# Optimization experiments

Hardware: AMD Instinct MI355X
Metric: run time of the kernel (lower is better)

Reference implementation:

```python
import jax, jax.numpy as jnp
import numpy as np

N = 100000
E = 1600000
F_IN = 128
HID = 128
C = 10
NEG_SLOPE = 0.2


def setup_inputs() -> dict:
    key = jax.random.key(0)
    ks = jax.random.split(key, 12)
    x = jax.random.normal(ks[0], (N, F_IN), dtype=jnp.float32)
    edge_index = jax.random.randint(ks[1], (2, E), 0, N, dtype=jnp.int64)
    batch = jnp.zeros((N,), dtype=jnp.int64)
    s1 = 1.0 / np.sqrt(F_IN)
    s2 = 1.0 / np.sqrt(HID)
    return {
        "x": x,
        "edge_index": edge_index,
        "batch": batch,
        "W1": jax.random.normal(ks[2], (F_IN, HID), dtype=jnp.float32) * s1,
        "a_src1": jax.random.normal(ks[3], (HID,), dtype=jnp.float32) * s2,
        "a_dst1": jax.random.normal(ks[4], (HID,), dtype=jnp.float32) * s2,
        "b1": jnp.zeros((HID,), dtype=jnp.float32),
        "W2": jax.random.normal(ks[5], (HID, HID), dtype=jnp.float32) * s2,
        "a_src2": jax.random.normal(ks[6], (HID,), dtype=jnp.float32) * s2,
        "a_dst2": jax.random.normal(ks[7], (HID,), dtype=jnp.float32) * s2,
        "b2": jnp.zeros((HID,), dtype=jnp.float32),
        "Wlin": jax.random.normal(ks[8], (HID, C), dtype=jnp.float32) * s2,
        "blin": jnp.zeros((C,), dtype=jnp.float32),
    }


def gat_conv(x, src, dst, W, a_src, a_dst, b):
    # PyG GATConv, heads=1: h = xW; alpha_e = softmax_dst(leaky_relu(a_src.h[src] + a_dst.h[dst]))
    h = x @ W                                  # [N, H]
    alpha_s = h @ a_src                        # [N]
    alpha_d = h @ a_dst                        # [N]
    e = jax.nn.leaky_relu(alpha_s[src] + alpha_d[dst], NEG_SLOPE)  # [E]
    m = jax.ops.segment_max(e, dst, num_segments=N)                # per-dst max (stable softmax)
    ex = jnp.exp(e - m[dst])
    denom = jax.ops.segment_sum(ex, dst, num_segments=N)
    alpha = ex / (denom[dst] + 1e-16)          # [E]
    out = jax.ops.segment_sum(h[src] * alpha[:, None], dst, num_segments=N)
    return out + b


def reference(x, edge_index, batch, W1, a_src1, a_dst1, b1, W2, a_src2, a_dst2, b2, Wlin, blin):
    x = x.astype(jnp.float32)
    loops = jnp.arange(N, dtype=edge_index.dtype)
    src = jnp.concatenate([edge_index[0], loops])  # add_self_loops=True
    dst = jnp.concatenate([edge_index[1], loops])
    h = jax.nn.relu(gat_conv(x, src, dst, W1, a_src1, a_dst1, b1))
    h = jax.nn.relu(gat_conv(h, src, dst, W2, a_src2, a_dst2, b2))
    # dropout(p=0.5) is identity in eval mode
    return h @ Wlin + blin
```

## Files before the change

kernel.cpp:

```cpp
#include <hip/hip_runtime.h>

#define N_NODES 100000
#define N_EDGES 1600000
#define TOTE    (N_EDGES + N_NODES)
#define NEG     0.2f
#define NB      ((N_NODES + 255) >> 8)
#define BCAP    5120

typedef __attribute__((ext_vector_type(8))) short bf16x8;
typedef __attribute__((ext_vector_type(4))) float floatx4;

__device__ __forceinline__ unsigned short f2bf(float f) {
  unsigned int u = __float_as_uint(f);
  u += 0x7fffu + ((u >> 16) & 1u);
  return (unsigned short)(u >> 16);
}
__device__ __forceinline__ float bf_lo(unsigned int r) { return __uint_as_float(r << 16); }
__device__ __forceinline__ float bf_hi(unsigned int r) { return __uint_as_float(r & 0xffff0000u); }

__global__ __launch_bounds__(256) void k_wprep(const float* __restrict__ W1, const float* __restrict__ W2,
                                               unsigned short* __restrict__ B1hi, unsigned short* __restrict__ B1lo,
                                               unsigned short* __restrict__ B2hi, unsigned short* __restrict__ B2lo,
                                               int* __restrict__ bucketCnt) {
  int b = blockIdx.x;
  int t = threadIdx.x;
  if (b == 16) {
    for (int i = t; i < NB * 16; i += 256) bucketCnt[i] = 0;
    return;
  }
  const float* W = (b < 8) ? W1 : W2;
  unsigned short* Bh = (b < 8) ? B1hi : B2hi;
  unsigned short* Bl = (b < 8) ? B1lo : B2lo;
  int ntile = b & 7;
  int kq = t >> 6, lane = t & 63;
  int q = lane >> 4, m = lane & 15;
  int n = ntile * 16 + m;
  union { unsigned short us[8]; uint4 u4; } hi, lo;
#pragma unroll
  for (int j = 0; j < 8; ++j) {
    int k = kq * 32 + q * 8 + j;
    float w = W[(size_t)k * 128 + n];
    unsigned int u = __float_as_uint(w);
    hi.us[j] = (unsigned short)(u >> 16);
    float res = w - __uint_as_float(u & 0xffff0000u);
    lo.us[j] = f2bf(res);
  }
  size_t fo = ((size_t)(ntile * 4 + kq) * 64 + lane) * 8;
  *reinterpret_cast<uint4*>(Bh + fo) = hi.u4;
  *reinterpret_cast<uint4*>(Bl + fo) = lo.u4;
}

__global__ __launch_bounds__(256) void k_binA(const int* __restrict__ ei, int* __restrict__ bucketCnt,
                                              unsigned int* __restrict__ binned) {
  __shared__ int hist[NB];
  __shared__ int cur[NB];
  int t = threadIdx.x;
  for (int b = t; b < NB; b += 256) hist[b] = 0;
  __syncthreads();
  unsigned int pk[16]; int bk[16];
#pragma unroll
  for (int j = 0; j < 16; ++j) {
    int idx = blockIdx.x * 4096 + j * 256 + t;
    if (idx < N_EDGES) {
      int s = ei[idx], d = ei[N_EDGES + idx];
      bk[j] = d >> 8;
      pk[j] = ((unsigned int)s << 8) | (unsigned int)(d & 255);
      atomicAdd(&hist[bk[j]], 1);
    } else bk[j] = -1;
  }
  __syncthreads();
  for (int b = t; b < NB; b += 256) {
    int h = hist[b];
    if (h) cur[b] = b * BCAP + atomicAdd(&bucketCnt[b * 16], h);
  }
  __syncthreads();
#pragma unroll
  for (int j = 0; j < 16; ++j) {
    if (bk[j] >= 0) {
      int pos = atomicAdd(&cur[bk[j]], 1);
      binned[pos] = pk[j];
    }
  }
}

__global__ __launch_bounds__(512) void k_bin_scan(const int* __restrict__ bucketCnt,
                                                  int* __restrict__ binOffs) {
  __shared__ int sc[512];
  int t = threadIdx.x;
  int v = (t < NB) ? bucketCnt[t * 16] : 0;
  sc[t] = v; __syncthreads();
  for (int off = 1; off < 512; off <<= 1) {
    int x = (t >= off) ? sc[t - off] : 0;
    __syncthreads();
    sc[t] += x;
    __syncthreads();
  }
  int excl = sc[t] - v;
  if (t <= NB) binOffs[t] = excl;
}

__global__ __launch_bounds__(256) void k_binB(const unsigned int* __restrict__ binned,
                                              const int* __restrict__ binOffs,
                                              int* __restrict__ offs, int* __restrict__ srcs) {
  __shared__ int cnt[256];
  __shared__ int sc[256];
  __shared__ int cur[256];
  int b = blockIdx.x;
  int t = threadIdx.x;
  int node0 = b << 8;
  int nNodes = min(256, N_NODES - node0);
  int cntE = binOffs[b + 1] - binOffs[b];
  int e0 = b * BCAP, e1 = e0 + cntE;
  int base = binOffs[b] + node0;

  cnt[t] = 0; __syncthreads();
  for (int i = e0 + t; i < e1; i += 256) atomicAdd(&cnt[binned[i] & 255u], 1);
  __syncthreads();

  int v = (t < nNodes) ? cnt[t] + 1 : 0;
  sc[t] = v; __syncthreads();
  for (int off = 1; off < 256; off <<= 1) {
    int x = (t >= off) ? sc[t - off] : 0;
    __syncthreads();
    sc[t] += x;
    __syncthreads();
  }
  int excl = sc[t] - v;
  if (t < nNodes) {
    offs[node0 + t] = base + excl;
    srcs[base + excl] = node0 + t;
  }
  cur[t] = excl + 1;
  __syncthreads();

  for (int i = e0 + t; i < e1; i += 256) {
    unsigned int e = binned[i];
    int j = (int)(e & 255u);
    int s = (int)(e >> 8);
    int p = atomicAdd(&cur[j], 1);
    srcs[base + p] = s;
  }
  if (b == 0 && t == 0) offs[N_NODES] = TOTE;
}

template <bool SPLIT>
__global__ __launch_bounds__(256) void k_gemm_mfma(const void* __restrict__ Aptr,
                                                   const unsigned short* __restrict__ Bhi,
                                                   const unsigned short* __restrict__ Blo,
                                                   unsigned short* __restrict__ Cb,
                                                   const float* __restrict__ avS, const float* __restrict__ avD,
                                                   float* __restrict__ aS, float* __restrict__ aD,
                                                   float* __restrict__ slotS, float* __restrict__ slotD) {
  __shared__ unsigned short sC[64 * 136];
  __shared__ float redS[64 * 4], redD[64 * 4];
  __shared__ float mS[64], mD[64];
  int t = threadIdx.x;
  int w = t >> 6, lane = t & 63;
  int q = lane >> 4, m = lane & 15;
  int rbase = blockIdx.x * 64;

  floatx4 acc[4][2];
#pragma unroll
  for (int mt = 0; mt < 4; ++mt)
#pragma unroll
    for (int nt = 0; nt < 2; ++nt) acc[mt][nt] = (floatx4){0.f, 0.f, 0.f, 0.f};

#pragma unroll
  for (int k0 = 0; k0 < 4; ++k0) {
    bf16x8 Bh[2], Bl[2], Ah[4], Al[4];
#pragma unroll
    for (int nt = 0; nt < 2; ++nt) {
      int ntg = w * 2 + nt;
      size_t fo = ((size_t)(ntg * 4 + k0) * 64 + lane) * 8;
      Bh[nt] = *reinterpret_cast<const bf16x8*>(Bhi + fo);
      Bl[nt] = *reinterpret_cast<const bf16x8*>(Blo + fo);
    }
#pragma unroll
    for (int mt = 0; mt < 4; ++mt) {
      int row = rbase + mt * 16 + m;
      row = min(row, N_NODES - 1);
      if constexpr (SPLIT) {
        const float* ap = (const float*)Aptr + (size_t)row * 128 + k0 * 32 + q * 8;
        float4 v0 = *reinterpret_cast<const float4*>(ap);
        float4 v1 = *reinterpret_cast<const float4*>(ap + 4);
        float av[8] = {v0.x, v0.y, v0.z, v0.w, v1.x, v1.y, v1.z, v1.w};
        union { unsigned short us[8]; bf16x8 v; } uh, ul;
#pragma unroll
        for (int j = 0; j < 8; ++j) {
          unsigned int u = __float_as_uint(av[j]);
          uh.us[j] = (unsigned short)(u >> 16);
          float res = av[j] - __uint_as_float(u & 0xffff0000u);
          ul.us[j] = f2bf(res);
        }
        Ah[mt] = uh.v; Al[mt] = ul.v;
      } else {
        const unsigned short* ap = (const unsigned short*)Aptr + (size_t)row * 128 + k0 * 32 + q * 8;
        Ah[mt] = *reinterpret_cast<const bf16x8*>(ap);
      }
    }
#pragma unroll
    for (int mt = 0; mt < 4; ++mt)
#pragma unroll
      for (int nt = 0; nt < 2; ++nt) {
        acc[mt][nt] = __builtin_amdgcn_mfma_f32_16x16x32_bf16(Ah[mt], Bh[nt], acc[mt][nt], 0, 0, 0);
        acc[mt][nt] = __builtin_amdgcn_mfma_f32_16x16x32_bf16(Ah[mt], Bl[nt], acc[mt][nt], 0, 0, 0);
        if constexpr (SPLIT)
          acc[mt][nt] = __builtin_amdgcn_mfma_f32_16x16x32_bf16(Al[mt], Bh[nt], acc[mt][nt], 0, 0, 0);
      }
  }

  float avs[2], avd[2];
#pragma unroll
  for (int nt = 0; nt < 2; ++nt) {
    int c = w * 32 + nt * 16 + m;
    avs[nt] = avS[c];
    avd[nt] = avD[c];
  }
#pragma unroll
  for (int mt = 0; mt < 4; ++mt)
#pragma unroll
    for (int r = 0; r < 4; ++r) {
      float ps = acc[mt][0][r] * avs[0] + acc[mt][1][r] * avs[1];
      float pd = acc[mt][0][r] * avd[0] + acc[mt][1][r] * avd[1];
      ps += __shfl_xor(ps, 1); pd += __shfl_xor(pd, 1);
      ps += __shfl_xor(ps, 2); pd += __shfl_xor(pd, 2);
      ps += __shfl_xor(ps, 4); pd += __shfl_xor(pd, 4);
      ps += __shfl_xor(ps, 8); pd += __shfl_xor(pd, 8);
      if (m == 0) {
        int rl = mt * 16 + q * 4 + r;
        redS[rl * 4 + w] = ps;
        redD[rl * 4 + w] = pd;
      }
    }

#pragma unroll
  for (int mt = 0; mt < 4; ++mt)
#pragma unroll
    for (int nt = 0; nt < 2; ++nt)
#pragma unroll
      for (int r = 0; r < 4; ++r) {
        int rl = mt * 16 + q * 4 + r;
        int cl = w * 32 + nt * 16 + m;
        sC[rl * 136 + cl] = f2bf(acc[mt][nt][r]);
      }
  __syncthreads();

#pragma unroll
  for (int i = 0; i < 4; ++i) {
    int idx = i * 256 + t;
    int rl = idx >> 4, kk = idx & 15;
    int gr = rbase + rl;
    if (gr < N_NODES)
      *reinterpret_cast<uint4*>(Cb + (size_t)gr * 128 + kk * 8) =
          *reinterpret_cast<const uint4*>(sC + rl * 136 + kk * 8);
  }

  if (t < 64) {
    int gr = rbase + t;
    bool ok = gr < N_NODES;
    float ps = redS[t * 4] + redS[t * 4 + 1] + redS[t * 4 + 2] + redS[t * 4 + 3];
    float pd = redD[t * 4] + redD[t * 4 + 1] + redD[t * 4 + 2] + redD[t * 4 + 3];
    if (ok) { aS[gr] = ps; aD[gr] = pd; }
    mS[t] = ok ? ps : -1e30f;
    mD[t] = ok ? pd : -1e30f;
  }
  __syncthreads();
#pragma unroll
  for (int off = 32; off > 0; off >>= 1) {
    if (t < off) { mS[t] = fmaxf(mS[t], mS[t + off]); mD[t] = fmaxf(mD[t], mD[t + off]); }
    __syncthreads();
  }
  if (t == 0) { slotS[blockIdx.x] = mS[0]; slotD[blockIdx.x] = mD[0]; }
}

__global__ __launch_bounds__(256) void k_gmax(const float* __restrict__ slotS,
                                              const float* __restrict__ slotD,
                                              int n, float* __restrict__ gMh) {
  __shared__ float sS[256], sD[256];
  int t = threadIdx.x;
  float ms = -1e30f, md = -1e30f;
  for (int i = t; i < n; i += 256) { ms = fmaxf(ms, slotS[i]); md = fmaxf(md, slotD[i]); }
  sS[t] = ms; sD[t] = md;
  __syncthreads();
#pragma unroll
  for (int off = 128; off > 0; off >>= 1) {
    if (t < off) { sS[t] = fmaxf(sS[t], sS[t + off]); sD[t] = fmaxf(sD[t], sD[t + off]); }
    __syncthreads();
  }
  if (t == 0) {
    float M = sS[0] + sD[0];
    gMh[0] = (M > 0.f) ? M : NEG * M;
  }
}

#define FMA8(E, R)                                     \
  do {                                                 \
    acc[0] += (E) * bf_lo((R).x); acc[1] += (E) * bf_hi((R).x); \
    acc[2] += (E) * bf_lo((R).y); acc[3] += (E) * bf_hi((R).y); \
    acc[4] += (E) * bf_lo((R).z); acc[5] += (E) * bf_hi((R).z); \
    acc[6] += (E) * bf_lo((R).w); acc[7] += (E) * bf_hi((R).w); \
  } while (0)

__global__ __launch_bounds__(256) void k_aggregate(const unsigned short* __restrict__ hb,
                                                   const float* __restrict__ aS,
                                                   const float* __restrict__ aD,
                                                   const int* __restrict__ offs,
                                                   const int* __restrict__ srcs,
                                                   const float* __restrict__ bias,
                                                   const float* __restrict__ gMh,
                                                   unsigned short* __restrict__ outb) {
  __shared__ float2 pairs[16 * 17];
  int t = threadIdx.x;
  int g = t >> 4;
  int l = t & 15;
  int dst = blockIdx.x * 16 + g;
  float Mh = gMh[0];
  int beg = offs[dst], end = offs[dst + 1];
  float adn = aD[dst];
  float denom = 0.f;
  float acc[8];
#pragma unroll
  for (int k = 0; k < 8; ++k) acc[k] = 0.f;
  const int pbase = g * 17;

  for (int chunk = beg; chunk < end; chunk += 16) {
    int i = chunk + l;
    float ex = 0.f; int s = 0;
    if (i < end) {
      s = srcs[i];
      float e = aS[s] + adn;
      e = (e > 0.f) ? e : NEG * e;
      ex = __expf(e - Mh);
    }
    denom += ex;
    pairs[pbase + l] = make_float2(ex, __int_as_float(s));
    int cnt = min(16, end - chunk);
    int j = 0;
    for (; j + 4 <= cnt; j += 4) {
      float2 p0 = pairs[pbase + j + 0];
      float2 p1 = pairs[pbase + j + 1];
      float2 p2 = pairs[pbase + j + 2];
      float2 p3 = pairs[pbase + j + 3];
      uint4 r0 = *reinterpret_cast<const uint4*>(hb + (size_t)__float_as_int(p0.y) * 128 + l * 8);
      uint4 r1 = *reinterpret_cast<const uint4*>(hb + (size_t)__float_as_int(p1.y) * 128 + l * 8);
      uint4 r2 = *reinterpret_cast<const uint4*>(hb + (size_t)__float_as_int(p2.y) * 128 + l * 8);
      uint4 r3 = *reinterpret_cast<const uint4*>(hb + (size_t)__float_as_int(p3.y) * 128 + l * 8);
      FMA8(p0.x, r0);
      FMA8(p1.x, r1);
      FMA8(p2.x, r2);
      FMA8(p3.x, r3);
    }
    for (; j < cnt; ++j) {
      float2 pp = pairs[pbase + j];
      uint4 r = *reinterpret_cast<const uint4*>(hb + (size_t)__float_as_int(pp.y) * 128 + l * 8);
      FMA8(pp.x, r);
    }
  }
  denom += __shfl_xor(denom, 1);
  denom += __shfl_xor(denom, 2);
  denom += __shfl_xor(denom, 4);
  denom += __shfl_xor(denom, 8);
  float inv = 1.f / (denom + 1e-16f);
  float4 b0 = *reinterpret_cast<const float4*>(bias + l * 8);
  float4 b1 = *reinterpret_cast<const float4*>(bias + l * 8 + 4);
  float o0 = fmaxf(acc[0] * inv + b0.x, 0.f), o1 = fmaxf(acc[1] * inv + b0.y, 0.f);
  float o2 = fmaxf(acc[2] * inv + b0.z, 0.f), o3 = fmaxf(acc[3] * inv + b0.w, 0.f);
  float o4 = fmaxf(acc[4] * inv + b1.x, 0.f), o5 = fmaxf(acc[5] * inv + b1.y, 0.f);
  float o6 = fmaxf(acc[6] * inv + b1.z, 0.f), o7 = fmaxf(acc[7] * inv + b1.w, 0.f);
  union { unsigned short us[8]; uint4 u4; } oo;
  oo.us[0] = f2bf(o0); oo.us[1] = f2bf(o1); oo.us[2] = f2bf(o2); oo.us[3] = f2bf(o3);
  oo.us[4] = f2bf(o4); oo.us[5] = f2bf(o5); oo.us[6] = f2bf(o6); oo.us[7] = f2bf(o7);
  *reinterpret_cast<uint4*>(outb + (size_t)dst * 128 + l * 8) = oo.u4;
}

#define UNPK(V, B)                                     \
  do {                                                 \
    h[(B)+0] = bf_lo((V).x); h[(B)+1] = bf_hi((V).x);  \
    h[(B)+2] = bf_lo((V).y); h[(B)+3] = bf_hi((V).y);  \
    h[(B)+4] = bf_lo((V).z); h[(B)+5] = bf_hi((V).z);  \
    h[(B)+6] = bf_lo((V).w); h[(B)+7] = bf_hi((V).w);  \
  } while (0)

__global__ __launch_bounds__(256) void k_linear(const unsigned short* __restrict__ hb,
                                                const float* __restrict__ Wl,
                                                const float* __restrict__ bl,
                                                float* __restrict__ out) {
  __shared__ float sWt[10 * 144];
  __shared__ float sbl[10];
  int t = threadIdx.x;
  if (t < 128) {
    int jj = t >> 5, ii = t & 31;
#pragma unroll
    for (int c = 0; c < 10; ++c) sWt[c * 144 + jj * 36 + ii] = Wl[t * 10 + c];
  }
  if (t < 10) sbl[t] = bl[t];
  __syncthreads();
  int node = blockIdx.x * 64 + (t >> 2);
  int j = t & 3;
  if (node >= N_NODES) return;
  const unsigned short* hrow = hb + (size_t)node * 128 + j * 32;
  uint4 v0 = *reinterpret_cast<const uint4*>(hrow);
  uint4 v1 = *reinterpret_cast<const uint4*>(hrow + 8);
  uint4 v2 = *reinterpret_cast<const uint4*>(hrow + 16);
  uint4 v3 = *reinterpret_cast<const uint4*>(hrow + 24);
  float h[32];
  UNPK(v0, 0); UNPK(v1, 8); UNPK(v2, 16); UNPK(v3, 24);
  float p[10];
#pragma unroll
  for (int c = 0; c < 10; ++c) {
    const float4* wp = reinterpret_cast<const float4*>(&sWt[c * 144 + j * 36]);
    float s = 0.f;
#pragma unroll
    for (int qq = 0; qq < 8; ++qq) {
      float4 wv = wp[qq];
      s += h[qq * 4 + 0] * wv.x + h[qq * 4 + 1] * wv.y + h[qq * 4 + 2] * wv.z + h[qq * 4 + 3] * wv.w;
    }
    p[c] = s;
  }
#pragma unroll
  for (int c = 0; c < 10; ++c) {
    p[c] += __shfl_xor(p[c], 1);
    p[c] += __shfl_xor(p[c], 2);
  }
  if (j == 0) {
    float* orow = out + (size_t)node * 10;
    *reinterpret_cast<float2*>(orow + 0) = make_float2(p[0] + sbl[0], p[1] + sbl[1]);
    *reinterpret_cast<float2*>(orow + 2) = make_float2(p[2] + sbl[2], p[3] + sbl[3]);
    *reinterpret_cast<float2*>(orow + 4) = make_float2(p[4] + sbl[4], p[5] + sbl[5]);
    *reinterpret_cast<float2*>(orow + 6) = make_float2(p[6] + sbl[6], p[7] + sbl[7]);
    *reinterpret_cast<float2*>(orow + 8) = make_float2(p[8] + sbl[8], p[9] + sbl[9]);
  }
}

extern "C" void kernel_launch(void* const* d_in, const int* in_sizes, int n_in,
                              void* d_out, int out_size, void* d_ws, size_t ws_size,
                              hipStream_t stream) {
  const float* x   = (const float*)d_in[0];
  const int*   ei  = (const int*)d_in[1];
  const float* W1  = (const float*)d_in[3];
  const float* as1 = (const float*)d_in[4];
  const float* ad1 = (const float*)d_in[5];
  const float* b1  = (const float*)d_in[6];
  const float* W2  = (const float*)d_in[7];
  const float* as2 = (const float*)d_in[8];
  const float* ad2 = (const float*)d_in[9];
  const float* b2  = (const float*)d_in[10];
  const float* Wl  = (const float*)d_in[11];
  const float* bl  = (const float*)d_in[12];
  float* out = (float*)d_out;

  char* p = (char*)d_ws;
  unsigned short* hb   = (unsigned short*)p; p += (size_t)N_NODES * 128 * sizeof(unsigned short);
  unsigned short* hagg = (unsigned short*)p; p += (size_t)N_NODES * 128 * sizeof(unsigned short);
  float* aS    = (float*)p; p += (size_t)N_NODES * sizeof(float);
  float* aD    = (float*)p; p += (size_t)N_NODES * sizeof(float);
  int* offs    = (int*)p;   p += (size_t)(N_NODES + 4) * sizeof(int);
  int* srcs    = (int*)p;   p += (size_t)TOTE * sizeof(int);
  int* bucketCnt = (int*)p; p += (size_t)NB * 16 * sizeof(int);
  int* binOffs   = (int*)p; p += (size_t)(NB + 4) * sizeof(int);
  float* slotS = (float*)p; p += 2048 * sizeof(float);
  float* slotD = (float*)p; p += 2048 * sizeof(float);
  float* gMh = (float*)p;   p += 4 * sizeof(float);
  unsigned short* B1hi = (unsigned short*)p; p += 128 * 128 * sizeof(unsigned short);
  unsigned short* B1lo = (unsigned short*)p; p += 128 * 128 * sizeof(unsigned short);
  unsigned short* B2hi = (unsigned short*)p; p += 128 * 128 * sizeof(unsigned short);
  unsigned short* B2lo = (unsigned short*)p; p += 128 * 128 * sizeof(unsigned short);
  unsigned int* binned = (unsigned int*)hagg;

  int binBlocks = (N_EDGES + 4095) / 4096;

  k_wprep<<<17, 256, 0, stream>>>(W1, W2, B1hi, B1lo, B2hi, B2lo, bucketCnt);
  k_binA<<<binBlocks, 256, 0, stream>>>(ei, bucketCnt, binned);
  k_bin_scan<<<1, 512, 0, stream>>>(bucketCnt, binOffs);
  k_binB<<<NB, 256, 0, stream>>>(binned, binOffs, offs, srcs);

  int gemmBlocks = (N_NODES + 63) / 64;
  int aggBlocks  = N_NODES / 16;
  int linBlocks  = (N_NODES + 63) / 64;

  k_gemm_mfma<true><<<gemmBlocks, 256, 0, stream>>>(x, B1hi, B1lo, hb, as1, ad1, aS, aD, slotS, slotD);
  k_gmax<<<1, 256, 0, stream>>>(slotS, slotD, gemmBlocks, gMh);
  k_aggregate<<<aggBlocks, 256, 0, stream>>>(hb, aS, aD, offs, srcs, b1, gMh, hagg);
  k_gemm_mfma<false><<<gemmBlocks, 256, 0, stream>>>(hagg, B2hi, B2lo, hb, as2, ad2, aS, aD, slotS, slotD);
  k_gmax<<<1, 256, 0, stream>>>(slotS, slotD, gemmBlocks, gMh);
  k_aggregate<<<aggBlocks, 256, 0, stream>>>(hb, aS, aD, offs, srcs, b2, gMh, hagg);
  k_linear<<<linBlocks, 256, 0, stream>>>(hagg, Wl, bl, out);
}
```

Measured before the change: 364.9 us.

## Store node features in column slices and aggregate each slice separately

Changes the bf16 hidden feature layout from row-major [N,128] to eight column slices of [N,16]. The GEMM writes and the second GEMM and linear stage read this layout. Aggregation runs as eight blocks per destination group, one per slice, so each slice's 3.2 MB working set can stay cached during random source gathers. Edge softmax weights are computed once in a separate k_exs pass and stored to global memory. This adds an extra kernel, extra edge traffic, and an 8x re-read of srcs/exs per slice.

```diff
diff --git a/kernel.cpp b/kernel.cpp
--- a/kernel.cpp
+++ b/kernel.cpp
@@ -6,6 +6,7 @@
 #define NEG     0.2f
 #define NB      ((N_NODES + 255) >> 8)
 #define BCAP    5120
+#define SLICE_STRIDE ((size_t)N_NODES * 16)
 
 typedef __attribute__((ext_vector_type(8))) short bf16x8;
 typedef __attribute__((ext_vector_type(4))) float floatx4;
@@ -194,7 +195,9 @@
         }
         Ah[mt] = uh.v; Al[mt] = ul.v;
       } else {
-        const unsigned short* ap = (const unsigned short*)Aptr + (size_t)row * 128 + k0 * 32 + q * 8;
+        int slice = 2 * k0 + (q >> 1);
+        const unsigned short* ap = (const unsigned short*)Aptr +
+            ((size_t)slice * N_NODES + row) * 16 + (q & 1) * 8;
         Ah[mt] = *reinterpret_cast<const bf16x8*>(ap);
       }
     }
@@ -245,14 +248,17 @@
       }
   __syncthreads();
 
-#pragma unroll
-  for (int i = 0; i < 4; ++i) {
-    int idx = i * 256 + t;
-    int rl = idx >> 4, kk = idx & 15;
-    int gr = rbase + rl;
-    if (gr < N_NODES)
-      *reinterpret_cast<uint4*>(Cb + (size_t)gr * 128 + kk * 8) =
-          *reinterpret_cast<const uint4*>(sC + rl * 136 + kk * 8);
+  {
+    int slice = t >> 5, sub = t & 31;
+    int rowoff = sub >> 1, half = sub & 1;
+#pragma unroll
+    for (int it = 0; it < 4; ++it) {
+      int rl = it * 16 + rowoff;
+      int gr = rbase + rl;
+      if (gr < N_NODES)
+        *reinterpret_cast<uint4*>(Cb + ((size_t)slice * N_NODES + gr) * 16 + half * 8) =
+            *reinterpret_cast<const uint4*>(sC + rl * 136 + slice * 16 + half * 8);
+    }
   }
 
   if (t < 64) {
@@ -293,7 +299,33 @@
   }
 }
 
-#define FMA8(E, R)                                     \
+__global__ __launch_bounds__(256) void k_exs(const float* __restrict__ aS, const float* __restrict__ aD,
+                                             const int* __restrict__ offs, const int* __restrict__ srcs,
+                                             const float* __restrict__ gMh,
+                                             float* __restrict__ exs, float* __restrict__ inv) {
+  int t = threadIdx.x;
+  int g = t >> 4, l = t & 15;
+  int dst = blockIdx.x * 16 + g;
+  float Mh = gMh[0];
+  int beg = offs[dst], end = offs[dst + 1];
+  float adn = aD[dst];
+  float denom = 0.f;
+  for (int i = beg + l; i < end; i += 16) {
+    int s = srcs[i];
+    float e = aS[s] + adn;
+    e = (e > 0.f) ? e : NEG * e;
+    float ex = __expf(e - Mh);
+    exs[i] = ex;
+    denom += ex;
+  }
+  denom += __shfl_xor(denom, 1);
+  denom += __shfl_xor(denom, 2);
+  denom += __shfl_xor(denom, 4);
+  denom += __shfl_xor(denom, 8);
+  if (l == 0) inv[dst] = 1.f / (denom + 1e-16f);
+}
+
+#define FMA8S(E, R)                                    \
   do {                                                 \
     acc[0] += (E) * bf_lo((R).x); acc[1] += (E) * bf_hi((R).x); \
     acc[2] += (E) * bf_lo((R).y); acc[3] += (E) * bf_hi((R).y); \
@@ -301,23 +333,22 @@
     acc[6] += (E) * bf_lo((R).w); acc[7] += (E) * bf_hi((R).w); \
   } while (0)
 
-__global__ __launch_bounds__(256) void k_aggregate(const unsigned short* __restrict__ hb,
-                                                   const float* __restrict__ aS,
-                                                   const float* __restrict__ aD,
+__global__ __launch_bounds__(256) void k_agg_slice(const unsigned short* __restrict__ hb_s,
                                                    const int* __restrict__ offs,
                                                    const int* __restrict__ srcs,
+                                                   const float* __restrict__ exs,
+                                                   const float* __restrict__ inv,
                                                    const float* __restrict__ bias,
-                                                   const float* __restrict__ gMh,
-                                                   unsigned short* __restrict__ outb) {
+                                                   unsigned short* __restrict__ out_s) {
   __shared__ float2 pairs[16 * 17];
   int t = threadIdx.x;
-  int g = t >> 4;
-  int l = t & 15;
-  int dst = blockIdx.x * 16 + g;
-  float Mh = gMh[0];
+  int g = t >> 4, l = t & 15;
+  int s = blockIdx.x & 7;
+  int grp = blockIdx.x >> 3;
+  int dst = grp * 16 + g;
   int beg = offs[dst], end = offs[dst + 1];
-  float adn = aD[dst];
-  float denom = 0.f;
+  int es = l >> 1, half = l & 1;
+  const unsigned short* base = hb_s + (size_t)s * SLICE_STRIDE + half * 8;
   float acc[8];
 #pragma unroll
   for (int k = 0; k < 8; ++k) acc[k] = 0.f;
@@ -325,52 +356,38 @@
 
   for (int chunk = beg; chunk < end; chunk += 16) {
     int i = chunk + l;
-    float ex = 0.f; int s = 0;
-    if (i < end) {
-      s = srcs[i];
-      float e = aS[s] + adn;
-      e = (e > 0.f) ? e : NEG * e;
-      ex = __expf(e - Mh);
-    }
-    denom += ex;
-    pairs[pbase + l] = make_float2(ex, __int_as_float(s));
+    float ex = 0.f; int sr = 0;
+    if (i < end) { sr = srcs[i]; ex = exs[i]; }
+    pairs[pbase + l] = make_float2(ex, __int_as_float(sr));
     int cnt = min(16, end - chunk);
-    int j = 0;
-    for (; j + 4 <= cnt; j += 4) {
-      float2 p0 = pairs[pbase + j + 0];
-      float2 p1 = pairs[pbase + j + 1];
-      float2 p2 = pairs[pbase + j + 2];
-      float2 p3 = pairs[pbase + j + 3];
-      uint4 r0 = *reinterpret_cast<const uint4*>(hb + (size_t)__float_as_int(p0.y) * 128 + l * 8);
-      uint4 r1 = *reinterpret_cast<const uint4*>(hb + (size_t)__float_as_int(p1.y) * 128 + l * 8);
-      uint4 r2 = *reinterpret_cast<const uint4*>(hb + (size_t)__float_as_int(p2.y) * 128 + l * 8);
-      uint4 r3 = *reinterpret_cast<const uint4*>(hb + (size_t)__float_as_int(p3.y) * 128 + l * 8);
-      FMA8(p0.x, r0);
-      FMA8(p1.x, r1);
-      FMA8(p2.x, r2);
-      FMA8(p3.x, r3);
-    }
-    for (; j < cnt; ++j) {
-      float2 pp = pairs[pbase + j];
-      uint4 r = *reinterpret_cast<const uint4*>(hb + (size_t)__float_as_int(pp.y) * 128 + l * 8);
-      FMA8(pp.x, r);
-    }
-  }
-  denom += __shfl_xor(denom, 1);
-  denom += __shfl_xor(denom, 2);
-  denom += __shfl_xor(denom, 4);
-  denom += __shfl_xor(denom, 8);
-  float inv = 1.f / (denom + 1e-16f);
-  float4 b0 = *reinterpret_cast<const float4*>(bias + l * 8);
-  float4 b1 = *reinterpret_cast<const float4*>(bias + l * 8 + 4);
-  float o0 = fmaxf(acc[0] * inv + b0.x, 0.f), o1 = fmaxf(acc[1] * inv + b0.y, 0.f);
-  float o2 = fmaxf(acc[2] * inv + b0.z, 0.f), o3 = fmaxf(acc[3] * inv + b0.w, 0.f);
-  float o4 = fmaxf(acc[4] * inv + b1.x, 0.f), o5 = fmaxf(acc[5] * inv + b1.y, 0.f);
-  float o6 = fmaxf(acc[6] * inv + b1.z, 0.f), o7 = fmaxf(acc[7] * inv + b1.w, 0.f);
-  union { unsigned short us[8]; uint4 u4; } oo;
-  oo.us[0] = f2bf(o0); oo.us[1] = f2bf(o1); oo.us[2] = f2bf(o2); oo.us[3] = f2bf(o3);
-  oo.us[4] = f2bf(o4); oo.us[5] = f2bf(o5); oo.us[6] = f2bf(o6); oo.us[7] = f2bf(o7);
-  *reinterpret_cast<uint4*>(outb + (size_t)dst * 128 + l * 8) = oo.u4;
+#pragma unroll
+    for (int it = 0; it < 2; ++it) {
+      int jj = it * 8 + es;
+      if (jj < cnt) {
+        float2 pp = pairs[pbase + jj];
+        uint4 r = *reinterpret_cast<const uint4*>(base + (size_t)__float_as_int(pp.y) * 16);
+        FMA8S(pp.x, r);
+      }
+    }
+  }
+#pragma unroll
+  for (int off = 2; off <= 8; off <<= 1) {
+#pragma unroll
+    for (int k = 0; k < 8; ++k) acc[k] += __shfl_xor(acc[k], off);
+  }
+  if (es == 0) {
+    float iv = inv[dst];
+    float4 b0 = *reinterpret_cast<const float4*>(bias + s * 16 + half * 8);
+    float4 b1 = *reinterpret_cast<const float4*>(bias + s * 16 + half * 8 + 4);
+    float o0 = fmaxf(acc[0] * iv + b0.x, 0.f), o1 = fmaxf(acc[1] * iv + b0.y, 0.f);
+    float o2 = fmaxf(acc[2] * iv + b0.z, 0.f), o3 = fmaxf(acc[3] * iv + b0.w, 0.f);
+    float o4 = fmaxf(acc[4] * iv + b1.x, 0.f), o5 = fmaxf(acc[5] * iv + b1.y, 0.f);
+    float o6 = fmaxf(acc[6] * iv + b1.z, 0.f), o7 = fmaxf(acc[7] * iv + b1.w, 0.f);
+    union { unsigned short us[8]; uint4 u4; } oo;
+    oo.us[0] = f2bf(o0); oo.us[1] = f2bf(o1); oo.us[2] = f2bf(o2); oo.us[3] = f2bf(o3);
+    oo.us[4] = f2bf(o4); oo.us[5] = f2bf(o5); oo.us[6] = f2bf(o6); oo.us[7] = f2bf(o7);
+    *reinterpret_cast<uint4*>(out_s + ((size_t)s * N_NODES + dst) * 16 + half * 8) = oo.u4;
+  }
 }
 
 #define UNPK(V, B)                                     \
@@ -381,7 +398,7 @@
     h[(B)+6] = bf_lo((V).w); h[(B)+7] = bf_hi((V).w);  \
   } while (0)
 
-__global__ __launch_bounds__(256) void k_linear(const unsigned short* __restrict__ hb,
+__global__ __launch_bounds__(256) void k_linear(const unsigned short* __restrict__ hb_s,
                                                 const float* __restrict__ Wl,
                                                 const float* __restrict__ bl,
                                                 float* __restrict__ out) {
@@ -398,11 +415,12 @@
   int node = blockIdx.x * 64 + (t >> 2);
   int j = t & 3;
   if (node >= N_NODES) return;
-  const unsigned short* hrow = hb + (size_t)node * 128 + j * 32;
-  uint4 v0 = *reinterpret_cast<const uint4*>(hrow);
-  uint4 v1 = *reinterpret_cast<const uint4*>(hrow + 8);
-  uint4 v2 = *reinterpret_cast<const uint4*>(hrow + 16);
-  uint4 v3 = *reinterpret_cast<const uint4*>(hrow + 24);
+  const unsigned short* h0 = hb_s + ((size_t)(2 * j) * N_NODES + node) * 16;
+  const unsigned short* h1 = hb_s + ((size_t)(2 * j + 1) * N_NODES + node) * 16;
+  uint4 v0 = *reinterpret_cast<const uint4*>(h0);
+  uint4 v1 = *reinterpret_cast<const uint4*>(h0 + 8);
+  uint4 v2 = *reinterpret_cast<const uint4*>(h1);
+  uint4 v3 = *reinterpret_cast<const uint4*>(h1 + 8);
   float h[32];
   UNPK(v0, 0); UNPK(v1, 8); UNPK(v2, 16); UNPK(v3, 24);
   float p[10];
@@ -454,6 +472,8 @@
   unsigned short* hagg = (unsigned short*)p; p += (size_t)N_NODES * 128 * sizeof(unsigned short);
   float* aS    = (float*)p; p += (size_t)N_NODES * sizeof(float);
   float* aD    = (float*)p; p += (size_t)N_NODES * sizeof(float);
+  float* exs   = (float*)p; p += (size_t)TOTE * sizeof(float);
+  float* inv   = (float*)p; p += (size_t)N_NODES * sizeof(float);
   int* offs    = (int*)p;   p += (size_t)(N_NODES + 4) * sizeof(int);
   int* srcs    = (int*)p;   p += (size_t)TOTE * sizeof(int);
   int* bucketCnt = (int*)p; p += (size_t)NB * 16 * sizeof(int);
@@ -475,14 +495,17 @@
   k_binB<<<NB, 256, 0, stream>>>(binned, binOffs, offs, srcs);
 
   int gemmBlocks = (N_NODES + 63) / 64;
-  int aggBlocks  = N_NODES / 16;
+  int dstBlocks  = N_NODES / 16;
+  int aggBlocks  = dstBlocks * 8;
   int linBlocks  = (N_NODES + 63) / 64;
 
   k_gemm_mfma<true><<<gemmBlocks, 256, 0, stream>>>(x, B1hi, B1lo, hb, as1, ad1, aS, aD, slotS, slotD);
   k_gmax<<<1, 256, 0, stream>>>(slotS, slotD, gemmBlocks, gMh);
-  k_aggregate<<<aggBlocks, 256, 0, stream>>>(hb, aS, aD, offs, srcs, b1, gMh, hagg);
+  k_exs<<<dstBlocks, 256, 0, stream>>>(aS, aD, offs, srcs, gMh, exs, inv);
+  k_agg_slice<<<aggBlocks, 256, 0, stream>>>(hb, offs, srcs, exs, inv, b1, hagg);
   k_gemm_mfma<false><<<gemmBlocks, 256, 0, stream>>>(hagg, B2hi, B2lo, hb, as2, ad2, aS, aD, slotS, slotD);
   k_gmax<<<1, 256, 0, stream>>>(slotS, slotD, gemmBlocks, gMh);
-  k_aggregate<<<aggBlocks, 256, 0, stream>>>(hb, aS, aD, offs, srcs, b2, gMh, hagg);
+  k_exs<<<dstBlocks, 256, 0, stream>>>(aS, aD, offs, srcs, gMh, exs, inv);
+  k_agg_slice<<<aggBlocks, 256, 0, stream>>>(hb, offs, srcs, exs, inv, b2, hagg);
   k_linear<<<linBlocks, 256, 0, stream>>>(hagg, Wl, bl, out);
 }
```

Measured after the change: 445.7 us. +22.1%, slower.
